# Kernel optimization log

Measured on AMD Instinct MI355X. Metric: run time of the kernel, lower is better.

## Reference

```python
import jax, jax.numpy as jnp
import numpy as np

B, T, E, H = 64, 50, 1024, 1024
NU, NI = 100000, 32000
K, W, N = 4, 32, 10  # vcov window, hcov kernel width, hcov out channels


def setup_inputs() -> dict:
    key = jax.random.key(0)
    ks = jax.random.split(key, 16)
    f = lambda k, shape, s=0.02: jax.random.normal(k, shape, jnp.float32) * s
    return {
        "user_vectors": jax.random.randint(ks[0], (B, T), 0, NU),
        "item_vectors": jax.random.randint(ks[1], (B, T), 0, NI),
        "user_emb": f(ks[2], (NU, E)),
        "item_emb": f(ks[3], (NI, E)),
        "att_W": f(ks[4], (H + 2 * E, E)),      # att_linear weight (in, out)
        "att_b": jnp.zeros((E,), jnp.float32),
        "W_ih": f(ks[5], (3 * H, 2 * E)),        # GRUCell input weights (r,z,n)
        "b_ih": jnp.zeros((3 * H,), jnp.float32),
        "W_hh": f(ks[6], (3 * H, H)),
        "b_hh": f(ks[7], (3 * H,), 0.01),
        "hcov_W": f(ks[8], (N, W)),              # Conv1d(1, n, w) kernel
        "hcov_b": f(ks[9], (N,), 0.01),
        "vcov_W": f(ks[10], (K,)),               # Conv1d(k, 1, 1) kernel
        "vcov_b": f(ks[11], (1,), 0.01),
        "lin_W": f(ks[12], (N + 2 * H, NI)),     # output Linear (in, out)
        "lin_b": jnp.zeros((NI,), jnp.float32),
    }


def reference(user_vectors, item_vectors, user_emb, item_emb, att_W, att_b,
              W_ih, b_ih, W_hh, b_hh, hcov_W, hcov_b, vcov_W, vcov_b,
              lin_W, lin_b):
    # dropout layers are identity in eval mode
    u = user_emb[user_vectors]   # (B,T,E)
    it = item_emb[item_vectors]  # (B,T,E)
    Wu, Wi, Wh = att_W[:E], att_W[E:2 * E], att_W[2 * E:]
    # precompute the input-dependent part of att_linear outside the scan
    att_pre = jnp.einsum('bte,ef->btf', u, Wu) + jnp.einsum('bte,ef->btf', it, Wi) + att_b
    Lout = H - W + 1  # hcov output length

    us = jnp.swapaxes(u, 0, 1)        # (T,B,E)
    its = jnp.swapaxes(it, 0, 1)
    ap = jnp.swapaxes(att_pre, 0, 1)
    idx = jnp.arange(T)

    h0 = jnp.zeros((B, H), u.dtype)
    buf0 = jnp.zeros((K, B, H), u.dtype)  # rolling buffer of last K hidden states

    def step(carry, inp):
        h, buf = carry
        a_pre, ut, itt, i = inp
        att = jax.nn.sigmoid(a_pre + h @ Wh)                 # (B,E)
        x = jnp.concatenate([att * ut, (1 - att) * itt], -1)  # (B,2E)
        # PyTorch GRUCell math (gate order r,z,n)
        gi = x @ W_ih.T + b_ih
        gh = h @ W_hh.T + b_hh
        r = jax.nn.sigmoid(gi[:, :H] + gh[:, :H])
        z = jax.nn.sigmoid(gi[:, H:2 * H] + gh[:, H:2 * H])
        n_ = jnp.tanh(gi[:, 2 * H:] + r * gh[:, 2 * H:])
        h = (1 - z) * n_ + z * h
        # sum over positions of Conv1d(1,N,W)(h) == sliding-window sums dot kernel
        csum = jnp.cumsum(h, -1)
        cs = csum[:, Lout - 1:] - jnp.pad(csum[:, :W - 1], ((0, 0), (1, 0)))  # (B,W)
        v = cs @ hcov_W.T + hcov_b * Lout                     # (B,N)
        # vcov: 1x1 conv over the K-stack of hidden states
        buf = jnp.concatenate([buf[1:], h[None]], 0)          # (K,B,H)
        q = jnp.einsum('c,cbh->bh', vcov_W, buf) + vcov_b
        l = jnp.where(i >= K - 1, h * q, jnp.zeros_like(h))
        return (h, buf), (v, h, l)

    _, (vs, hs, ls) = jax.lax.scan(step, (h0, buf0), (ap, us, its, idx))
    ful = jnp.concatenate([jnp.swapaxes(vs, 0, 1),
                           jnp.swapaxes(hs, 0, 1),
                           jnp.swapaxes(ls, 0, 1)], -1)  # (B,T,N+2H)
    logits = ful @ lin_W + lin_b                          # (B,T,NI)
    return jax.nn.log_softmax(logits, -1)
```

## Files before the change

kernel.cpp:

```cpp
#include <hip/hip_runtime.h>
#include <cstdint>
#include <cstddef>

#define B_    64
#define T_    50
#define E_    1024
#define H_    1024
#define NI_   32000
#define KF_   2058
#define KP_   2080
#define NW_   10
#define LOUT_ 993.0f

typedef __bf16 bf16_t;
typedef __bf16 bf16x4 __attribute__((ext_vector_type(4)));
typedef __bf16 bf16x8 __attribute__((ext_vector_type(8)));
typedef float  f32x4  __attribute__((ext_vector_type(4)));

#define MFMA16(a,b,c) __builtin_amdgcn_mfma_f32_16x16x32_bf16((a),(b),(c),0,0,0)

__global__ __launch_bounds__(256) void k_init(float* hs0, bf16_t* h0bf) {
    int i = blockIdx.x * 256 + threadIdx.x;
    if (i < B_ * H_) { hs0[i] = 0.f; h0bf[i] = (bf16_t)0.f; }
}

__global__ __launch_bounds__(256)
void k_gather(const int* __restrict__ uv, const int* __restrict__ iv,
              const float* __restrict__ uemb, const float* __restrict__ iemb,
              bf16_t* __restrict__ Abuf) {
    int row = blockIdx.x;
    int tid = threadIdx.x;
    int uid = uv[row], iid = iv[row];
    float4 a = ((const float4*)(uemb + (size_t)uid * E_))[tid];
    float4 b = ((const float4*)(iemb + (size_t)iid * E_))[tid];
    bf16_t* dst = Abuf + (size_t)row * 2048;
    bf16x4 va; va[0]=(bf16_t)a.x; va[1]=(bf16_t)a.y; va[2]=(bf16_t)a.z; va[3]=(bf16_t)a.w;
    bf16x4 vb; vb[0]=(bf16_t)b.x; vb[1]=(bf16_t)b.y; vb[2]=(bf16_t)b.z; vb[3]=(bf16_t)b.w;
    *(bf16x4*)(dst + tid * 4) = va;
    *(bf16x4*)(dst + 1024 + tid * 4) = vb;
}

__global__ __launch_bounds__(256)
void k_transpose_bf16(const float* __restrict__ in, bf16_t* __restrict__ out,
                      int K, int Nn, int Kout) {
    __shared__ float tile[32][33];
    int kb = blockIdx.x * 32, nb = blockIdx.y * 32;
    int tx = threadIdx.x & 31, ty = threadIdx.x >> 5;
#pragma unroll
    for (int r = 0; r < 32; r += 8) {
        int k = kb + ty + r, n = nb + tx;
        float v = (k < K && n < Nn) ? in[(size_t)k * Nn + n] : 0.f;
        tile[ty + r][tx] = v;
    }
    __syncthreads();
#pragma unroll
    for (int r = 0; r < 32; r += 8) {
        int n = nb + ty + r, k = kb + tx;
        if (n < Nn && k < Kout) out[(size_t)n * Kout + k] = (bf16_t)tile[tx][ty + r];
    }
}

__global__ __launch_bounds__(256)
void k_cvt(const float* __restrict__ in, bf16_t* __restrict__ out, int n) {
    int i = (blockIdx.x * 256 + threadIdx.x) * 4;
    if (i + 3 < n) {
        float4 v = *(const float4*)(in + i);
        bf16x4 o; o[0]=(bf16_t)v.x; o[1]=(bf16_t)v.y; o[2]=(bf16_t)v.z; o[3]=(bf16_t)v.w;
        *(bf16x4*)(out + i) = o;
    }
}

__global__ __launch_bounds__(256)
void k_gemm_bt(const bf16_t* __restrict__ A, int lda,
               const bf16_t* __restrict__ Bt, int ldb,
               const float* __restrict__ bias,
               float* __restrict__ C, int ldc, int K) {
    __shared__ bf16_t As[128][40];
    __shared__ bf16_t Bs[128][40];
    int m0 = blockIdx.x * 128, n0 = blockIdx.y * 128;
    int tid = threadIdx.x, lane = tid & 63, wave = tid >> 6;
    int wm = (wave & 1) * 64, wn = (wave >> 1) * 64;
    int quad = lane >> 4, l16 = lane & 15;
    f32x4 acc[4][4] = {};
    for (int k0 = 0; k0 < K; k0 += 32) {
        __syncthreads();
#pragma unroll
        for (int c = tid; c < 512; c += 256) {
            int row = c >> 2, kc = (c & 3) * 8;
            *(bf16x8*)&As[row][kc] = *(const bf16x8*)(A + (size_t)(m0 + row) * lda + k0 + kc);
            *(bf16x8*)&Bs[row][kc] = *(const bf16x8*)(Bt + (size_t)(n0 + row) * ldb + k0 + kc);
        }
        __syncthreads();
        bf16x8 af[4], bf[4];
#pragma unroll
        for (int mt = 0; mt < 4; mt++) af[mt] = *(bf16x8*)&As[wm + mt * 16 + l16][quad * 8];
#pragma unroll
        for (int nt = 0; nt < 4; nt++) bf[nt] = *(bf16x8*)&Bs[wn + nt * 16 + l16][quad * 8];
#pragma unroll
        for (int mt = 0; mt < 4; mt++)
#pragma unroll
            for (int nt = 0; nt < 4; nt++)
                acc[mt][nt] = MFMA16(af[mt], bf[nt], acc[mt][nt]);
    }
#pragma unroll
    for (int mt = 0; mt < 4; mt++)
#pragma unroll
        for (int nt = 0; nt < 4; nt++) {
            int col = n0 + wn + nt * 16 + l16;
            float bv = bias ? bias[col] : 0.f;
#pragma unroll
            for (int r = 0; r < 4; r++) {
                int row = m0 + wm + mt * 16 + quad * 4 + r;
                C[(size_t)row * ldc + col] = acc[mt][nt][r] + bv;
            }
        }
}

__global__ __launch_bounds__(256)
void k_att_step(const bf16_t* __restrict__ Hcur,
                const bf16_t* __restrict__ WhT,
                int ldwh,
                const float* __restrict__ att_pre,
                const bf16_t* __restrict__ Abuf,
                bf16_t* __restrict__ Xb,
                int t) {
    __shared__ float red[4][64][16];
    int tid = threadIdx.x, lane = tid & 63, wave = tid >> 6;
    int quad = lane >> 4, l16 = lane & 15;
    int c0 = blockIdx.x * 16;
    f32x4 acc[4] = {};
    int kbase = wave * 256;
#pragma unroll
    for (int kk = 0; kk < 256; kk += 32) {
        int k = kbase + kk + quad * 8;
        bf16x8 bf = *(const bf16x8*)(WhT + (size_t)(c0 + l16) * ldwh + k);
#pragma unroll
        for (int mt = 0; mt < 4; mt++) {
            bf16x8 af = *(const bf16x8*)(Hcur + (size_t)(mt * 16 + l16) * 1024 + k);
            acc[mt] = MFMA16(af, bf, acc[mt]);
        }
    }
#pragma unroll
    for (int mt = 0; mt < 4; mt++)
#pragma unroll
        for (int r = 0; r < 4; r++)
            red[wave][mt * 16 + quad * 4 + r][l16] = acc[mt][r];
    __syncthreads();
    for (int i = tid; i < 1024; i += 256) {
        int m = i >> 4, c = i & 15;
        float s = red[0][m][c] + red[1][m][c] + red[2][m][c] + red[3][m][c];
        int col = c0 + c;
        int arow = m * T_ + t;
        float att = 1.f / (1.f + __expf(-(att_pre[(size_t)arow * 1024 + col] + s)));
        float uvv = (float)Abuf[(size_t)arow * 2048 + col];
        float ivv = (float)Abuf[(size_t)arow * 2048 + 1024 + col];
        Xb[(size_t)m * 2048 + col] = (bf16_t)(att * uvv);
        Xb[(size_t)m * 2048 + 1024 + col] = (bf16_t)((1.f - att) * ivv);
    }
}

__global__ __launch_bounds__(256)
void k_gates_step(const bf16_t* __restrict__ Xb,
                  const bf16_t* __restrict__ Hcur,
                  const bf16_t* __restrict__ Wih,
                  const bf16_t* __restrict__ Whh,
                  const float* __restrict__ b_ih, const float* __restrict__ b_hh,
                  const float* __restrict__ hprev,
                  float* __restrict__ hout,
                  bf16_t* __restrict__ Hnxt) {
    __shared__ float red[8][64][16];
    int tid = threadIdx.x, lane = tid & 63, wave = tid >> 6;
    int quad = lane >> 4, l16 = lane & 15;
    int c0 = blockIdx.x * 16;
    f32x4 a0[4] = {}, a1[4] = {};
    int s0, s1;
    if (wave < 2) {
        int kb = wave * 1024;
#pragma unroll 4
        for (int kk = 0; kk < 1024; kk += 32) {
            int k = kb + kk + quad * 8;
            bf16x8 br = *(const bf16x8*)(Wih + (size_t)(c0 + l16) * 2048 + k);
            bf16x8 bz = *(const bf16x8*)(Wih + (size_t)(1024 + c0 + l16) * 2048 + k);
#pragma unroll
            for (int mt = 0; mt < 4; mt++) {
                bf16x8 af = *(const bf16x8*)(Xb + (size_t)(mt * 16 + l16) * 2048 + k);
                a0[mt] = MFMA16(af, br, a0[mt]);
                a1[mt] = MFMA16(af, bz, a1[mt]);
            }
        }
        s0 = wave; s1 = 3 + wave;
    } else if (wave == 2) {
#pragma unroll 4
        for (int kk = 0; kk < 1024; kk += 32) {
            int k = kk + quad * 8;
            bf16x8 br = *(const bf16x8*)(Whh + (size_t)(c0 + l16) * 1024 + k);
            bf16x8 bz = *(const bf16x8*)(Whh + (size_t)(1024 + c0 + l16) * 1024 + k);
#pragma unroll
            for (int mt = 0; mt < 4; mt++) {
                bf16x8 af = *(const bf16x8*)(Hcur + (size_t)(mt * 16 + l16) * 1024 + k);
                a0[mt] = MFMA16(af, br, a0[mt]);
                a1[mt] = MFMA16(af, bz, a1[mt]);
            }
        }
        s0 = 2; s1 = 5;
    } else {
#pragma unroll 4
        for (int kk = 0; kk < 2048; kk += 32) {
            int k = kk + quad * 8;
            bf16x8 bn = *(const bf16x8*)(Wih + (size_t)(2048 + c0 + l16) * 2048 + k);
#pragma unroll
            for (int mt = 0; mt < 4; mt++) {
                bf16x8 af = *(const bf16x8*)(Xb + (size_t)(mt * 16 + l16) * 2048 + k);
                a0[mt] = MFMA16(af, bn, a0[mt]);
            }
        }
#pragma unroll 4
        for (int kk = 0; kk < 1024; kk += 32) {
            int k = kk + quad * 8;
            bf16x8 bn = *(const bf16x8*)(Whh + (size_t)(2048 + c0 + l16) * 1024 + k);
#pragma unroll
            for (int mt = 0; mt < 4; mt++) {
                bf16x8 af = *(const bf16x8*)(Hcur + (size_t)(mt * 16 + l16) * 1024 + k);
                a1[mt] = MFMA16(af, bn, a1[mt]);
            }
        }
        s0 = 6; s1 = 7;
    }
#pragma unroll
    for (int mt = 0; mt < 4; mt++)
#pragma unroll
        for (int r = 0; r < 4; r++) {
            red[s0][mt * 16 + quad * 4 + r][l16] = a0[mt][r];
            red[s1][mt * 16 + quad * 4 + r][l16] = a1[mt][r];
        }
    __syncthreads();
    for (int i = tid; i < 1024; i += 256) {
        int m = i >> 4, c = i & 15;
        int gc = c0 + c;
        float rsum = red[0][m][c] + red[1][m][c] + red[2][m][c] + b_ih[gc] + b_hh[gc];
        float zsum = red[3][m][c] + red[4][m][c] + red[5][m][c] + b_ih[1024 + gc] + b_hh[1024 + gc];
        float gin = red[6][m][c] + b_ih[2048 + gc];
        float ghn = red[7][m][c] + b_hh[2048 + gc];
        float rr = 1.f / (1.f + __expf(-rsum));
        float zz = 1.f / (1.f + __expf(-zsum));
        float nn = tanhf(gin + rr * ghn);
        float hold = hprev[(size_t)m * 1024 + gc];
        float hnew = (1.f - zz) * nn + zz * hold;
        hout[(size_t)m * 1024 + gc] = hnew;
        Hnxt[(size_t)m * 1024 + gc] = (bf16_t)hnew;
    }
}

__global__ __launch_bounds__(256)
void k_post(const float* __restrict__ hs,
            const float* __restrict__ hcovW, const float* __restrict__ hcovb,
            const float* __restrict__ vcovW, const float* __restrict__ vcovb,
            bf16_t* __restrict__ ful) {
    int row = blockIdx.x;
    int b = row / T_, t = row % T_;
    const float* h = hs + ((size_t)(t + 1) * 64 + b) * 1024;
    __shared__ float sh[1024];
    __shared__ float wsum[4];
    __shared__ float cs[32];
    int tid = threadIdx.x;
    float4 hv = ((const float4*)h)[tid];
    sh[tid * 4 + 0] = hv.x; sh[tid * 4 + 1] = hv.y;
    sh[tid * 4 + 2] = hv.z; sh[tid * 4 + 3] = hv.w;
    float local = hv.x + hv.y + hv.z + hv.w;
#pragma unroll
    for (int off = 32; off; off >>= 1) local += __shfl_down(local, off);
    if ((tid & 63) == 0) wsum[tid >> 6] = local;
    __syncthreads();
    float total = wsum[0] + wsum[1] + wsum[2] + wsum[3];
    if (tid < 32) {
        float p = 0.f;
        for (int i = 0; i < tid; i++) p += sh[i];
        float s = 0.f;
        for (int i = 993 + tid; i < 1024; i++) s += sh[i];
        cs[tid] = total - p - s;
    }
    __syncthreads();
    bf16_t* outr = ful + (size_t)row * KP_;
    if (tid < NW_) {
        float v = hcovb[tid] * LOUT_;
        for (int j = 0; j < 32; j++) v += cs[j] * hcovW[tid * 32 + j];
        outr[tid] = (bf16_t)v;
    }
    if (tid < (KP_ - KF_)) outr[KF_ + tid] = (bf16_t)0.f;
    float vb = vcovb[0];
    for (int i = tid; i < 1024; i += 256) {
        float hh = sh[i];
        outr[NW_ + i] = (bf16_t)hh;
        float l = 0.f;
        if (t >= 3) {
            float q = vb;
#pragma unroll
            for (int c = 0; c < 4; c++)
                q += vcovW[c] * hs[((size_t)(t - 3 + c + 1) * 64 + b) * 1024 + i];
            l = hh * q;
        }
        outr[NW_ + 1024 + i] = (bf16_t)l;
    }
}

__global__ __launch_bounds__(256)
void k_logsoftmax(float* __restrict__ logits) {
    int row = blockIdx.x;
    float* p = logits + (size_t)row * NI_;
    int tid = threadIdx.x;
    __shared__ float red[4];
    float mx = -1e30f;
    for (int c = tid; c < NI_ / 4; c += 256) {
        float4 v = ((const float4*)p)[c];
        mx = fmaxf(mx, fmaxf(fmaxf(v.x, v.y), fmaxf(v.z, v.w)));
    }
#pragma unroll
    for (int off = 32; off; off >>= 1) mx = fmaxf(mx, __shfl_down(mx, off));
    if ((tid & 63) == 0) red[tid >> 6] = mx;
    __syncthreads();
    mx = fmaxf(fmaxf(red[0], red[1]), fmaxf(red[2], red[3]));
    __syncthreads();
    float s = 0.f;
    for (int c = tid; c < NI_ / 4; c += 256) {
        float4 v = ((const float4*)p)[c];
        s += __expf(v.x - mx) + __expf(v.y - mx) + __expf(v.z - mx) + __expf(v.w - mx);
    }
#pragma unroll
    for (int off = 32; off; off >>= 1) s += __shfl_down(s, off);
    if ((tid & 63) == 0) red[tid >> 6] = s;
    __syncthreads();
    s = red[0] + red[1] + red[2] + red[3];
    float lse = mx + __logf(s);
    for (int c = tid; c < NI_ / 4; c += 256) {
        float4 v = ((const float4*)p)[c];
        v.x -= lse; v.y -= lse; v.z -= lse; v.w -= lse;
        ((float4*)p)[c] = v;
    }
}

extern "C" void kernel_launch(void* const* d_in, const int* in_sizes, int n_in,
                              void* d_out, int out_size, void* d_ws, size_t ws_size,
                              hipStream_t stream) {
    const int*   uv    = (const int*)d_in[0];
    const int*   iv    = (const int*)d_in[1];
    const float* uemb  = (const float*)d_in[2];
    const float* iemb  = (const float*)d_in[3];
    const float* attW  = (const float*)d_in[4];
    const float* attb  = (const float*)d_in[5];
    const float* Wih   = (const float*)d_in[6];
    const float* bih   = (const float*)d_in[7];
    const float* Whh   = (const float*)d_in[8];
    const float* bhh   = (const float*)d_in[9];
    const float* hcovW = (const float*)d_in[10];
    const float* hcovb = (const float*)d_in[11];
    const float* vcovW = (const float*)d_in[12];
    const float* vcovb = (const float*)d_in[13];
    const float* linW  = (const float*)d_in[14];
    const float* linb  = (const float*)d_in[15];
    float* out = (float*)d_out;

    char* p = (char*)d_ws;
    auto alloc = [&](size_t bytes) { void* r = (void*)p; p += (bytes + 255) & ~(size_t)255; return r; };
    bf16_t* Abuf   = (bf16_t*)alloc((size_t)3200 * 2048 * 2);
    float*  attpre = (float*) alloc((size_t)3200 * 1024 * 4);
    bf16_t* attWt  = (bf16_t*)alloc((size_t)1024 * 3072 * 2);
    bf16_t* WihB   = (bf16_t*)alloc((size_t)3072 * 2048 * 2);
    bf16_t* WhhB   = (bf16_t*)alloc((size_t)3072 * 1024 * 2);
    bf16_t* linWt  = (bf16_t*)alloc((size_t)32000 * KP_ * 2);
    bf16_t* fulB   = (bf16_t*)alloc((size_t)3200 * KP_ * 2);
    float*  hsB    = (float*) alloc((size_t)51 * 64 * 1024 * 4);
    bf16_t* Xb     = (bf16_t*)alloc((size_t)64 * 2048 * 2);
    bf16_t* Hbf    = (bf16_t*)alloc((size_t)2 * 64 * 1024 * 2);

    k_init<<<256, 256, 0, stream>>>(hsB, Hbf);
    k_gather<<<3200, 256, 0, stream>>>(uv, iv, uemb, iemb, Abuf);
    k_transpose_bf16<<<dim3(96, 32), 256, 0, stream>>>(attW, attWt, 3072, 1024, 3072);
    k_transpose_bf16<<<dim3(65, 1000), 256, 0, stream>>>(linW, linWt, KF_, NI_, KP_);
    k_cvt<<<6144, 256, 0, stream>>>(Wih, WihB, 3072 * 2048);
    k_cvt<<<3072, 256, 0, stream>>>(Whh, WhhB, 3072 * 1024);
    k_gemm_bt<<<dim3(25, 8), 256, 0, stream>>>(Abuf, 2048, attWt, 3072, attb, attpre, 1024, 2048);
    bf16_t* Hcur = Hbf;
    bf16_t* Hnxt = Hbf + 64 * 1024;
    for (int t = 0; t < T_; t++) {
        k_att_step<<<64, 256, 0, stream>>>(Hcur, attWt + 2048, 3072, attpre, Abuf, Xb, t);
        k_gates_step<<<64, 256, 0, stream>>>(Xb, Hcur, WihB, WhhB, bih, bhh,
                                             hsB + (size_t)t * 65536,
                                             hsB + (size_t)(t + 1) * 65536, Hnxt);
        bf16_t* tmp = Hcur; Hcur = Hnxt; Hnxt = tmp;
    }
    k_post<<<3200, 256, 0, stream>>>(hsB, hcovW, hcovb, vcovW, vcovb, fulB);
    k_gemm_bt<<<dim3(25, 250), 256, 0, stream>>>(fulB, KP_, linWt, KP_, linb, out, NI_, KP_);
    k_logsoftmax<<<3200, 256, 0, stream>>>(out);
}
```

Before: 4.516 ms.

## Use direct global-to-LDS loads, XCD-aware block remap, and online logsoftmax

The GEMM now stages A/B tiles with global_load_lds 16-byte direct copies into unpadded LDS tiles instead of register round-trips. It also remaps workgroup IDs so consecutive tiles land on the same XCD for L2 reuse. Separately, logsoftmax fuses its max and sum passes into a single online pass, cutting one full read of the logits. Dropping the LDS padding may add bank conflicts on the fragment reads. The online softmax adds extra exp calls whenever the running max changes.

```diff
diff --git a/kernel.cpp b/kernel.cpp
--- a/kernel.cpp
+++ b/kernel.cpp
@@ -18,6 +18,9 @@
 typedef float  f32x4  __attribute__((ext_vector_type(4)));
 
 #define MFMA16(a,b,c) __builtin_amdgcn_mfma_f32_16x16x32_bf16((a),(b),(c),0,0,0)
+
+typedef const __attribute__((address_space(1))) void* gptr_t;
+typedef __attribute__((address_space(3))) void*       lptr_t;
 
 __global__ __launch_bounds__(256) void k_init(float* hs0, bf16_t* h0bf) {
     int i = blockIdx.x * 256 + threadIdx.x;
@@ -70,32 +73,54 @@
     }
 }
 
+__device__ inline void xcd_remap(int& mblk, int& nblk) {
+    int gx = gridDim.x;
+    int nwg = gx * gridDim.y;
+    int flat = blockIdx.x + gx * blockIdx.y;
+    int q = nwg >> 3, r = nwg & 7;
+    int xcd = flat & 7, seq = flat >> 3;
+    int base = (xcd < r) ? xcd * (q + 1) : r * (q + 1) + (xcd - r) * q;
+    int g = base + seq;
+    mblk = g % gx;
+    nblk = g / gx;
+}
+
 __global__ __launch_bounds__(256)
 void k_gemm_bt(const bf16_t* __restrict__ A, int lda,
                const bf16_t* __restrict__ Bt, int ldb,
                const float* __restrict__ bias,
                float* __restrict__ C, int ldc, int K) {
-    __shared__ bf16_t As[128][40];
-    __shared__ bf16_t Bs[128][40];
-    int m0 = blockIdx.x * 128, n0 = blockIdx.y * 128;
+    __shared__ __attribute__((aligned(16))) bf16_t As[128 * 32];
+    __shared__ __attribute__((aligned(16))) bf16_t Bs[128 * 32];
+    int mblk, nblk;
+    xcd_remap(mblk, nblk);
+    int m0 = mblk * 128, n0 = nblk * 128;
     int tid = threadIdx.x, lane = tid & 63, wave = tid >> 6;
     int wm = (wave & 1) * 64, wn = (wave >> 1) * 64;
     int quad = lane >> 4, l16 = lane & 15;
+    int c0 = wave * 2;
+    int srow = lane >> 2, scol = (lane & 3) * 8;
+    const bf16_t* gA0 = A  + (size_t)(m0 + c0 * 16      + srow) * lda + scol;
+    const bf16_t* gA1 = A  + (size_t)(m0 + c0 * 16 + 16 + srow) * lda + scol;
+    const bf16_t* gB0 = Bt + (size_t)(n0 + c0 * 16      + srow) * ldb + scol;
+    const bf16_t* gB1 = Bt + (size_t)(n0 + c0 * 16 + 16 + srow) * ldb + scol;
+    bf16_t* lA0 = As + c0 * 512;
+    bf16_t* lA1 = As + c0 * 512 + 512;
+    bf16_t* lB0 = Bs + c0 * 512;
+    bf16_t* lB1 = Bs + c0 * 512 + 512;
     f32x4 acc[4][4] = {};
     for (int k0 = 0; k0 < K; k0 += 32) {
         __syncthreads();
-#pragma unroll
-        for (int c = tid; c < 512; c += 256) {
-            int row = c >> 2, kc = (c & 3) * 8;
-            *(bf16x8*)&As[row][kc] = *(const bf16x8*)(A + (size_t)(m0 + row) * lda + k0 + kc);
-            *(bf16x8*)&Bs[row][kc] = *(const bf16x8*)(Bt + (size_t)(n0 + row) * ldb + k0 + kc);
-        }
+        __builtin_amdgcn_global_load_lds((gptr_t)(gA0 + k0), (lptr_t)lA0, 16, 0, 0);
+        __builtin_amdgcn_global_load_lds((gptr_t)(gA1 + k0), (lptr_t)lA1, 16, 0, 0);
+        __builtin_amdgcn_global_load_lds((gptr_t)(gB0 + k0), (lptr_t)lB0, 16, 0, 0);
+        __builtin_amdgcn_global_load_lds((gptr_t)(gB1 + k0), (lptr_t)lB1, 16, 0, 0);
         __syncthreads();
         bf16x8 af[4], bf[4];
 #pragma unroll
-        for (int mt = 0; mt < 4; mt++) af[mt] = *(bf16x8*)&As[wm + mt * 16 + l16][quad * 8];
-#pragma unroll
-        for (int nt = 0; nt < 4; nt++) bf[nt] = *(bf16x8*)&Bs[wn + nt * 16 + l16][quad * 8];
+        for (int mt = 0; mt < 4; mt++) af[mt] = *(bf16x8*)&As[(wm + mt * 16 + l16) * 32 + quad * 8];
+#pragma unroll
+        for (int nt = 0; nt < 4; nt++) bf[nt] = *(bf16x8*)&Bs[(wn + nt * 16 + l16) * 32 + quad * 8];
 #pragma unroll
         for (int mt = 0; mt < 4; mt++)
 #pragma unroll
@@ -308,29 +333,27 @@
     int row = blockIdx.x;
     float* p = logits + (size_t)row * NI_;
     int tid = threadIdx.x;
-    __shared__ float red[4];
-    float mx = -1e30f;
+    __shared__ float redm[4], reds[4];
+    float m = -1e30f, s = 0.f;
     for (int c = tid; c < NI_ / 4; c += 256) {
         float4 v = ((const float4*)p)[c];
-        mx = fmaxf(mx, fmaxf(fmaxf(v.x, v.y), fmaxf(v.z, v.w)));
-    }
-#pragma unroll
-    for (int off = 32; off; off >>= 1) mx = fmaxf(mx, __shfl_down(mx, off));
-    if ((tid & 63) == 0) red[tid >> 6] = mx;
-    __syncthreads();
-    mx = fmaxf(fmaxf(red[0], red[1]), fmaxf(red[2], red[3]));
-    __syncthreads();
-    float s = 0.f;
-    for (int c = tid; c < NI_ / 4; c += 256) {
-        float4 v = ((const float4*)p)[c];
-        s += __expf(v.x - mx) + __expf(v.y - mx) + __expf(v.z - mx) + __expf(v.w - mx);
-    }
-#pragma unroll
-    for (int off = 32; off; off >>= 1) s += __shfl_down(s, off);
-    if ((tid & 63) == 0) red[tid >> 6] = s;
-    __syncthreads();
-    s = red[0] + red[1] + red[2] + red[3];
-    float lse = mx + __logf(s);
+        float m4 = fmaxf(fmaxf(v.x, v.y), fmaxf(v.z, v.w));
+        if (m4 > m) { s *= __expf(m - m4); m = m4; }
+        s += __expf(v.x - m) + __expf(v.y - m) + __expf(v.z - m) + __expf(v.w - m);
+    }
+#pragma unroll
+    for (int off = 32; off; off >>= 1) {
+        float mo = __shfl_down(m, off), so = __shfl_down(s, off);
+        float mn = fmaxf(m, mo);
+        s = s * __expf(m - mn) + so * __expf(mo - mn);
+        m = mn;
+    }
+    if ((tid & 63) == 0) { redm[tid >> 6] = m; reds[tid >> 6] = s; }
+    __syncthreads();
+    float M = fmaxf(fmaxf(redm[0], redm[1]), fmaxf(redm[2], redm[3]));
+    float S = reds[0] * __expf(redm[0] - M) + reds[1] * __expf(redm[1] - M) +
+              reds[2] * __expf(redm[2] - M) + reds[3] * __expf(redm[3] - M);
+    float lse = M + __logf(S);
     for (int c = tid; c < NI_ / 4; c += 256) {
         float4 v = ((const float4*)p)[c];
         v.x -= lse; v.y -= lse; v.z -= lse; v.w -= lse;
```

Measured after the change: 4.274 ms. -5.4%, faster.
